# Optimization experiments

Measured on AMD Instinct MI355X. Metric: run time of the kernel, lower is better.

The kernel has to match this reference:

```python
import jax, jax.numpy as jnp
import numpy as np

HIDDEN = 2048
NUM_HEADS = 16
Q_LORA = 1536
KV_LORA = 512
QK_NOPE = 128
QK_ROPE = 64
V_HEAD = 128
EPS = 1e-6
QK_HEAD = QK_NOPE + QK_ROPE  # 192


def rmsnorm(x, w, eps=EPS):
    xf = x.astype(jnp.float32)
    var = jnp.mean(xf * xf, axis=-1, keepdims=True)
    return (w * (xf * jax.lax.rsqrt(var + eps)).astype(x.dtype))


def setup_inputs() -> dict:
    key = jax.random.key(0)
    ks = jax.random.split(key, 8)
    B, S = 1, 2048
    hidden_states = jax.random.normal(ks[0], (B, S, HIDDEN), dtype=jnp.float32)
    # causal additive mask [B,1,S,S]
    causal = jnp.tril(jnp.ones((S, S), dtype=bool))
    attention_mask = jnp.where(causal, 0.0, -1e9).astype(jnp.float32)[None, None]
    s = lambda fan_in: 1.0 / np.sqrt(fan_in)
    Wqa = jax.random.normal(ks[1], (HIDDEN, Q_LORA), dtype=jnp.float32) * s(HIDDEN)
    gqa = jnp.ones((Q_LORA,), dtype=jnp.float32)
    Wqb = jax.random.normal(ks[2], (Q_LORA, NUM_HEADS * QK_HEAD), dtype=jnp.float32) * s(Q_LORA)
    Wkva = jax.random.normal(ks[3], (HIDDEN, KV_LORA + QK_ROPE), dtype=jnp.float32) * s(HIDDEN)
    gkva = jnp.ones((KV_LORA,), dtype=jnp.float32)
    Wkvb = jax.random.normal(ks[4], (KV_LORA, NUM_HEADS * (QK_NOPE + V_HEAD)), dtype=jnp.float32) * s(KV_LORA)
    Wo = jax.random.normal(ks[5], (NUM_HEADS * V_HEAD, HIDDEN), dtype=jnp.float32) * s(NUM_HEADS * V_HEAD)
    return {"hidden_states": hidden_states, "attention_mask": attention_mask,
            "Wqa": Wqa, "gqa": gqa, "Wqb": Wqb, "Wkva": Wkva, "gkva": gkva,
            "Wkvb": Wkvb, "Wo": Wo}


def reference(hidden_states, attention_mask, Wqa, gqa, Wqb, Wkva, gkva, Wkvb, Wo):
    B, S, _ = hidden_states.shape
    # Q path: low-rank down-proj + RMSNorm + up-proj
    q_c = rmsnorm(hidden_states @ Wqa, gqa)
    q = (q_c @ Wqb).reshape(B, S, NUM_HEADS, QK_HEAD).transpose(0, 2, 1, 3)  # [B,H,S,192]
    # KV path: joint down-proj, split latent and shared rope part
    kv_c = hidden_states @ Wkva  # [B,S,KV_LORA+ROPE]
    kv_a, k_rope = kv_c[..., :KV_LORA], kv_c[..., KV_LORA:]
    kv = (rmsnorm(kv_a, gkva) @ Wkvb).reshape(B, S, NUM_HEADS, QK_NOPE + V_HEAD)
    k_nope, v = kv[..., :QK_NOPE], kv[..., QK_NOPE:]
    # shared rope part broadcast across heads (no rotary actually applied in source)
    k_rope_b = jnp.broadcast_to(k_rope[:, :, None, :], (B, S, NUM_HEADS, QK_ROPE))
    k = jnp.concatenate([k_nope, k_rope_b], axis=-1).transpose(0, 2, 1, 3)  # [B,H,S,192]
    v = v.transpose(0, 2, 1, 3)  # [B,H,S,128]
    scale = 1.0 / np.sqrt(QK_HEAD)
    attn = jnp.einsum("bhqd,bhkd->bhqk", q, k) * scale
    attn = attn + attention_mask
    attn = jax.nn.softmax(attn.astype(jnp.float32), axis=-1).astype(v.dtype)
    out = jnp.einsum("bhqk,bhkd->bhqd", attn, v)  # [B,H,S,128]
    out = out.transpose(0, 2, 1, 3).reshape(B, S, NUM_HEADS * V_HEAD)
    return out @ Wo
```

## Files before the change

kernel.cpp:

```cpp
#include <hip/hip_runtime.h>
#include <hip/hip_bf16.h>

typedef __bf16 bf16;
typedef __bf16 bf16x8 __attribute__((ext_vector_type(8)));
typedef __bf16 bf16x4 __attribute__((ext_vector_type(4)));
typedef float f32x4 __attribute__((ext_vector_type(4)));

#define HIDDEN 2048
#define SEQ 2048
#define NH 16
#define QL 1536
#define KVL 512
#define SCALE_LOG2E 0.10411754631f

__device__ __forceinline__ void gload_lds16(const void* g, void* l) {
  typedef const __attribute__((address_space(1))) void* gp_t;
  typedef __attribute__((address_space(3))) void* lp_t;
  __builtin_amdgcn_global_load_lds((gp_t)(unsigned long long)g,
                                   (lp_t)(unsigned int)(unsigned long long)l, 16, 0, 0);
}

__device__ __forceinline__ float fexp2(float x) {
  float r; asm("v_exp_f32 %0, %1" : "=v"(r) : "v"(x)); return r;
}
__device__ __forceinline__ unsigned cvt_pk_bf16(float lo, float hi) {
  unsigned r; asm("v_cvt_pk_bf16_f32 %0, %1, %2" : "=v"(r) : "v"(lo), "v"(hi)); return r;
}

__global__ void k_prep(const float* __restrict__ hidden, bf16* __restrict__ Xb,
                       const float* __restrict__ Wqa, bf16* __restrict__ WqaT,
                       const float* __restrict__ Wqb, bf16* __restrict__ WqbT,
                       const float* __restrict__ Wkva, bf16* __restrict__ WkvaT,
                       const float* __restrict__ Wkvb, bf16* __restrict__ WkvbT,
                       const float* __restrict__ Wo, bf16* __restrict__ WoT) {
  __shared__ float tile[32][33];
  int b = blockIdx.x, tid = threadIdx.x;
  const float* W; bf16* Wt; int K, N, bx, by;
  if (b < 3072)       { W = Wqa;  Wt = WqaT;  K = 2048; N = 1536; int r = b;         bx = r % 48;  by = r / 48; }
  else if (b < 7680)  { W = Wqb;  Wt = WqbT;  K = 1536; N = 3072; int r = b - 3072;  bx = r % 96;  by = r / 96; }
  else if (b < 8832)  { W = Wkva; Wt = WkvaT; K = 2048; N = 576;  int r = b - 7680;  bx = r % 18;  by = r / 18; }
  else if (b < 10880) { W = Wkvb; Wt = WkvbT; K = 512;  N = 4096; int r = b - 8832;  bx = r % 128; by = r / 128; }
  else if (b < 14976) { W = Wo;   Wt = WoT;   K = 2048; N = 2048; int r = b - 10880; bx = r % 64;  by = r / 64; }
  else {
    int r = b - 14976;
    int base = (r * 256 + tid) * 4;
    float4 v = *(const float4*)(hidden + base);
    bf16x4 o = { (bf16)v.x, (bf16)v.y, (bf16)v.z, (bf16)v.w };
    *(bf16x4*)(Xb + base) = o;
    return;
  }
  int n0 = bx * 32, k0 = by * 32, cc = tid & 31, rr = tid >> 5;
#pragma unroll
  for (int it = 0; it < 4; ++it) {
    int r = it * 8 + rr;
    tile[r][cc] = W[(size_t)(k0 + r) * N + n0 + cc];
  }
  __syncthreads();
#pragma unroll
  for (int it = 0; it < 4; ++it) {
    int r = it * 8 + rr;
    Wt[(size_t)(n0 + r) * K + k0 + cc] = (bf16)tile[cc][r];
  }
}

__device__ __forceinline__ void gemm_body(const bf16* __restrict__ A, const bf16* __restrict__ Bt,
                                          bf16* __restrict__ Cb, float* __restrict__ Cf,
                                          int N, int K, int m0, int n0, bf16* As, bf16* Bs) {
  int tid = threadIdx.x, lane = tid & 63, w = tid >> 6;
  int wr = w >> 1, wc = w & 1;
  int l15 = lane & 15, l4 = lane >> 4;
  f32x4 acc[4][4] = {};
  for (int k0 = 0; k0 < K; k0 += 64) {
#pragma unroll
    for (int i = 0; i < 4; ++i) {
      int c = w * 4 + i;
      int row = c * 8 + (lane >> 3);
      int col = (lane & 7) * 8;
      gload_lds16(&A[(size_t)(m0 + row) * K + k0 + col], &As[c * 512]);
      gload_lds16(&Bt[(size_t)(n0 + row) * K + k0 + col], &Bs[c * 512]);
    }
    __syncthreads();
#pragma unroll
    for (int kk = 0; kk < 2; ++kk) {
      bf16x8 af[4], bfr[4];
#pragma unroll
      for (int m = 0; m < 4; ++m)
        af[m] = *(const bf16x8*)&As[(wr * 64 + m * 16 + l15) * 64 + kk * 32 + l4 * 8];
#pragma unroll
      for (int n = 0; n < 4; ++n)
        bfr[n] = *(const bf16x8*)&Bs[(wc * 64 + n * 16 + l15) * 64 + kk * 32 + l4 * 8];
      __builtin_amdgcn_s_setprio(1);
#pragma unroll
      for (int m = 0; m < 4; ++m)
#pragma unroll
        for (int n = 0; n < 4; ++n)
          acc[m][n] = __builtin_amdgcn_mfma_f32_16x16x32_bf16(af[m], bfr[n], acc[m][n], 0, 0, 0);
      __builtin_amdgcn_s_setprio(0);
    }
    __syncthreads();
  }
#pragma unroll
  for (int m = 0; m < 4; ++m)
#pragma unroll
    for (int n = 0; n < 4; ++n)
#pragma unroll
      for (int r = 0; r < 4; ++r) {
        int grow = m0 + wr * 64 + m * 16 + l4 * 4 + r;
        int gcol = n0 + wc * 64 + n * 16 + l15;
        if (gcol < N) {
          float v = acc[m][n][r];
          if (Cf) Cf[(size_t)grow * N + gcol] = v;
          else Cb[(size_t)grow * N + gcol] = (bf16)v;
        }
      }
}

__global__ __launch_bounds__(256) void k_gemm(const bf16* __restrict__ A, const bf16* __restrict__ Bt,
                                              bf16* __restrict__ Cb, float* __restrict__ Cf,
                                              int N, int K) {
  __shared__ __align__(16) bf16 As[128 * 64];
  __shared__ __align__(16) bf16 Bs[128 * 64];
  gemm_body(A, Bt, Cb, Cf, N, K, blockIdx.x * 128, blockIdx.y * 128, As, Bs);
}

__global__ __launch_bounds__(256) void k_gemm_a(const bf16* __restrict__ Xb,
                                                const bf16* __restrict__ B1, const bf16* __restrict__ B2,
                                                float* __restrict__ C1, float* __restrict__ C2) {
  __shared__ __align__(16) bf16 As[128 * 64];
  __shared__ __align__(16) bf16 Bs[128 * 64];
  int by = blockIdx.y;
  if (by < 12) gemm_body(Xb, B1, nullptr, C1, 1536, 2048, blockIdx.x * 128, by * 128, As, Bs);
  else         gemm_body(Xb, B2, nullptr, C2, 576, 2048, blockIdx.x * 128, (by - 12) * 128, As, Bs);
}

__global__ __launch_bounds__(256) void k_gemm_b(const bf16* __restrict__ A1, const bf16* __restrict__ A2,
                                                const bf16* __restrict__ B1, const bf16* __restrict__ B2,
                                                bf16* __restrict__ C1, bf16* __restrict__ C2) {
  __shared__ __align__(16) bf16 As[128 * 64];
  __shared__ __align__(16) bf16 Bs[128 * 64];
  int by = blockIdx.y;
  if (by < 24) gemm_body(A1, B1, C1, nullptr, 3072, 1536, blockIdx.x * 128, by * 128, As, Bs);
  else         gemm_body(A2, B2, C2, nullptr, 4096, 512, blockIdx.x * 128, (by - 24) * 128, As, Bs);
}

__device__ inline float block_reduce_sum(float v, float* red) {
#pragma unroll
  for (int off = 1; off < 64; off <<= 1) v += __shfl_xor(v, off);
  int w = threadIdx.x >> 6;
  if ((threadIdx.x & 63) == 0) red[w] = v;
  __syncthreads();
  return red[0] + red[1] + red[2] + red[3];
}

__global__ void k_rms_all(const float* __restrict__ qa, const float* __restrict__ gq, bf16* __restrict__ qc,
                          const float* __restrict__ kvc, const float* __restrict__ gkv,
                          bf16* __restrict__ kvn, bf16* __restrict__ kr) {
  __shared__ float red[4];
  int b = blockIdx.x, tid = threadIdx.x;
  if (b < 2048) {
    int row = b;
    float v[6];
    float ss = 0.f;
#pragma unroll
    for (int j = 0; j < 6; ++j) {
      v[j] = qa[(size_t)row * QL + tid + j * 256];
      ss += v[j] * v[j];
    }
    float tot = block_reduce_sum(ss, red);
    float rs = rsqrtf(tot / (float)QL + 1e-6f);
#pragma unroll
    for (int j = 0; j < 6; ++j) {
      int c = tid + j * 256;
      qc[(size_t)row * QL + c] = (bf16)(v[j] * rs * gq[c]);
    }
  } else {
    int row = b - 2048;
    float v0 = kvc[(size_t)row * 576 + tid];
    float v1 = kvc[(size_t)row * 576 + tid + 256];
    float tot = block_reduce_sum(v0 * v0 + v1 * v1, red);
    float rs = rsqrtf(tot / (float)KVL + 1e-6f);
    kvn[(size_t)row * KVL + tid] = (bf16)(v0 * rs * gkv[tid]);
    kvn[(size_t)row * KVL + tid + 256] = (bf16)(v1 * rs * gkv[tid + 256]);
    if (tid < 64) kr[row * 64 + tid] = (bf16)kvc[(size_t)row * 576 + 512 + tid];
  }
}

__global__ void k_vt(const bf16* __restrict__ KVm, bf16* __restrict__ VT) {
  __shared__ bf16 tile[32][34];
  int b = blockIdx.x, tid = threadIdx.x;
  int h = b >> 8, rem = b & 255;
  int d0 = (rem >> 6) * 32, s0 = (rem & 63) * 32;
  int cc = tid & 31, rr = tid >> 5;
#pragma unroll
  for (int it = 0; it < 4; ++it) {
    int r = it * 8 + rr;
    tile[r][cc] = KVm[(size_t)(s0 + r) * 4096 + h * 256 + 128 + d0 + cc];
  }
  __syncthreads();
#pragma unroll
  for (int it = 0; it < 4; ++it) {
    int r = it * 8 + rr;
    VT[((size_t)(h * 128 + d0 + r)) * 2048 + s0 + cc] = tile[cc][r];
  }
}

__global__ __launch_bounds__(256) void k_attn(const bf16* __restrict__ Q, const bf16* __restrict__ KV,
                                              const bf16* __restrict__ KR, const bf16* __restrict__ VT,
                                              bf16* __restrict__ O) {
  __shared__ __align__(16) bf16 Ks[64 * 192];
  __shared__ __align__(16) bf16 Vt[128 * 64];
  __shared__ __align__(16) bf16 Ps[4 * 16 * 64];
  int bid = blockIdx.x;
  int h = bid & 15, i = bid >> 4;
  int qb = (i < 16) ? i : 47 - i;
  int q0 = qb * 64;
  int tid = threadIdx.x, lane = tid & 63, w = tid >> 6;
  int l15 = lane & 15, l4 = lane >> 4;
  int sw = (l15 & 7) << 4;
  char* PTw = (char*)Ps + w * 2048;
  const bf16* VTh = VT + (size_t)h * 128 * 2048;

  bf16x8 aq[6];
  int qrow = q0 + w * 16 + l15;
#pragma unroll
  for (int ks = 0; ks < 6; ++ks)
    aq[ks] = *(const bf16x8*)&Q[(size_t)qrow * 3072 + h * 192 + ks * 32 + l4 * 8];

  f32x4 oacc[8] = {};
  float mrun = -1e30f, lrun = 0.f;
  int nt = qb + 1;
  for (int t = 0; t < nt; ++t) {
#pragma unroll
    for (int it = 0; it < 6; ++it) {
      int idx = it * 256 + tid;
      int r = idx / 24, gg = idx - r * 24;
      int c = gg ^ (r & 7);
      const bf16* src = (c < 16) ? &KV[(size_t)(t * 64 + r) * 4096 + h * 256 + c * 8]
                                 : &KR[(size_t)(t * 64 + r) * 64 + (c - 16) * 8];
      gload_lds16(src, (char*)Ks + (it * 256 + w * 64) * 16);
    }
#pragma unroll
    for (int it = 0; it < 4; ++it) {
      int idx = it * 256 + tid;
      int d = idx >> 3, cc = idx & 7, c = cc ^ (d & 7);
      gload_lds16(&VTh[(size_t)d * 2048 + t * 64 + c * 8], (char*)Vt + (it * 256 + w * 64) * 16);
    }
    __syncthreads();

    f32x4 sacc[4] = {};
    __builtin_amdgcn_s_setprio(1);
#pragma unroll
    for (int ks = 0; ks < 6; ++ks) {
      int co = (((ks << 2) + l4) << 4) ^ sw;
#pragma unroll
      for (int n = 0; n < 4; ++n) {
        bf16x8 ak = *(const bf16x8*)((char*)Ks + (n * 16 + l15) * 384 + co);
        sacc[n] = __builtin_amdgcn_mfma_f32_16x16x32_bf16(ak, aq[ks], sacc[n], 0, 0, 0);
      }
    }
    __builtin_amdgcn_s_setprio(0);

    bool maskt = (t == qb);
#pragma unroll
    for (int n = 0; n < 4; ++n)
#pragma unroll
      for (int r = 0; r < 4; ++r) {
        float v = sacc[n][r] * SCALE_LOG2E;
        if (maskt) {
          int kvp = t * 64 + n * 16 + l4 * 4 + r;
          if (kvp > qrow) v = -1e30f;
        }
        sacc[n][r] = v;
      }

    float mx = sacc[0][0];
#pragma unroll
    for (int n = 0; n < 4; ++n)
#pragma unroll
      for (int r = 0; r < 4; ++r) mx = fmaxf(mx, sacc[n][r]);
    mx = fmaxf(mx, __shfl_xor(mx, 16));
    mx = fmaxf(mx, __shfl_xor(mx, 32));
    if (__any(mx - mrun > 8.0f)) {
      float mn = fmaxf(mrun, mx);
      float al = fexp2(mrun - mn);
      mrun = mn;
      lrun *= al;
#pragma unroll
      for (int vf = 0; vf < 8; ++vf) oacc[vf] *= al;
    }
    float rsum = 0.f;
#pragma unroll
    for (int n = 0; n < 4; ++n) {
      float e0 = fexp2(sacc[n][0] - mrun);
      float e1 = fexp2(sacc[n][1] - mrun);
      float e2 = fexp2(sacc[n][2] - mrun);
      float e3 = fexp2(sacc[n][3] - mrun);
      rsum += (e0 + e1) + (e2 + e3);
      uint2 u;
      u.x = cvt_pk_bf16(e0, e1);
      u.y = cvt_pk_bf16(e2, e3);
      *(uint2*)(PTw + l15 * 128 + ((n * 32 + l4 * 8) ^ sw)) = u;
    }
    rsum += __shfl_xor(rsum, 16);
    rsum += __shfl_xor(rsum, 32);
    lrun += rsum;

    __builtin_amdgcn_s_setprio(1);
#pragma unroll
    for (int ks = 0; ks < 2; ++ks) {
      int co = (((ks << 2) + l4) << 4) ^ sw;
      bf16x8 ap = *(const bf16x8*)(PTw + l15 * 128 + co);
#pragma unroll
      for (int vf = 0; vf < 8; ++vf) {
        bf16x8 av = *(const bf16x8*)((char*)Vt + (vf * 16 + l15) * 128 + co);
        oacc[vf] = __builtin_amdgcn_mfma_f32_16x16x32_bf16(av, ap, oacc[vf], 0, 0, 0);
      }
    }
    __builtin_amdgcn_s_setprio(0);
    __syncthreads();
  }

  char* OTw = (char*)Ks + w * 4096;
  float inv = 1.0f / lrun;
#pragma unroll
  for (int vf = 0; vf < 8; ++vf) {
    unsigned ua = cvt_pk_bf16(oacc[vf][0] * inv, oacc[vf][1] * inv);
    unsigned ub = cvt_pk_bf16(oacc[vf][2] * inv, oacc[vf][3] * inv);
    int base = vf * 32 + l4 * 8;
    *(unsigned*)(OTw + l15 * 256 + ((base + 0) ^ sw)) = ua;
    *(unsigned*)(OTw + l15 * 256 + ((base + 4) ^ sw)) = ub;
  }
  int qq = lane >> 2, c0 = lane & 3;
  size_t obase = (size_t)(q0 + w * 16 + qq) * 2048 + h * 128;
#pragma unroll
  for (int ii = 0; ii < 4; ++ii) {
    int ck = ii * 4 + c0;
    bf16x8 v = *(const bf16x8*)(OTw + qq * 256 + ((ck * 16) ^ ((qq & 7) << 4)));
    *(bf16x8*)&O[obase + ck * 8] = v;
  }
}

extern "C" void kernel_launch(void* const* d_in, const int* in_sizes, int n_in,
                              void* d_out, int out_size, void* d_ws, size_t ws_size,
                              hipStream_t stream) {
  (void)in_sizes; (void)n_in; (void)out_size; (void)ws_size;
  const float* hidden = (const float*)d_in[0];
  const float* Wqa  = (const float*)d_in[2];
  const float* gqa  = (const float*)d_in[3];
  const float* Wqb  = (const float*)d_in[4];
  const float* Wkva = (const float*)d_in[5];
  const float* gkva = (const float*)d_in[6];
  const float* Wkvb = (const float*)d_in[7];
  const float* Wo   = (const float*)d_in[8];
  float* out = (float*)d_out;

  char* ws = (char*)d_ws;
  size_t off = 0;
  auto alloc = [&](size_t bytes) {
    char* p = ws + off;
    off += (bytes + 255) & ~(size_t)255;
    return p;
  };
  bf16* Xb     = (bf16*)alloc((size_t)SEQ * HIDDEN * 2);
  bf16* WqaT   = (bf16*)alloc((size_t)QL * HIDDEN * 2);
  bf16* WqbT   = (bf16*)alloc((size_t)3072 * QL * 2);
  bf16* WkvaT  = (bf16*)alloc((size_t)576 * HIDDEN * 2);
  bf16* WkvbT  = (bf16*)alloc((size_t)4096 * KVL * 2);
  bf16* WoT    = (bf16*)alloc((size_t)2048 * 2048 * 2);
  float* qa    = (float*)alloc((size_t)SEQ * QL * 4);
  float* kvc   = (float*)alloc((size_t)SEQ * 576 * 4);
  bf16* qc     = (bf16*)alloc((size_t)SEQ * QL * 2);
  bf16* kvn    = (bf16*)alloc((size_t)SEQ * KVL * 2);
  bf16* krope  = (bf16*)alloc((size_t)SEQ * 64 * 2);
  bf16* Qm     = (bf16*)alloc((size_t)SEQ * 3072 * 2);
  bf16* KVm    = (bf16*)alloc((size_t)SEQ * 4096 * 2);
  bf16* VTg    = (bf16*)alloc((size_t)NH * 128 * SEQ * 2);
  bf16* Om     = (bf16*)alloc((size_t)SEQ * 2048 * 2);

  k_prep<<<19072, 256, 0, stream>>>(hidden, Xb, Wqa, WqaT, Wqb, WqbT,
                                    Wkva, WkvaT, Wkvb, WkvbT, Wo, WoT);
  k_gemm_a<<<dim3(16, 17), 256, 0, stream>>>(Xb, WqaT, WkvaT, qa, kvc);
  k_rms_all<<<4096, 256, 0, stream>>>(qa, gqa, qc, kvc, gkva, kvn, krope);
  k_gemm_b<<<dim3(16, 56), 256, 0, stream>>>(qc, kvn, WqbT, WkvbT, Qm, KVm);
  k_vt<<<4096, 256, 0, stream>>>(KVm, VTg);
  k_attn<<<512, 256, 0, stream>>>(Qm, KVm, krope, VTg, Om);
  k_gemm<<<dim3(16, 16), 256, 0, stream>>>(Om, WoT, nullptr, out, 2048, 2048);
}
```

Measured before the change: 236.5 us.

## Split attention KV range across blocks with 128-row query tiles and combine kernel

The attention kernel now processes 128 query rows per block, two 16-row groups per wave, so each K tile loaded into shared memory is reused twice as much. Longer causal query blocks are split along the KV dimension into 2-4 chunks (split-KV). Each chunk writes its unnormalized partial output and per-row max/sum, and a new combine kernel merges them with log-sum-exp weights. This is meant to cut K/V load traffic and balance work across the 640 blocks. The cost is an extra kernel launch, partial outputs rounded to bf16, and more register pressure from the doubled accumulators.

```diff
diff --git a/kernel.cpp b/kernel.cpp
--- a/kernel.cpp
+++ b/kernel.cpp
@@ -206,30 +206,38 @@
 
 __global__ __launch_bounds__(256) void k_attn(const bf16* __restrict__ Q, const bf16* __restrict__ KV,
                                               const bf16* __restrict__ KR, const bf16* __restrict__ VT,
-                                              bf16* __restrict__ O) {
+                                              bf16* __restrict__ O,
+                                              bf16* __restrict__ Opart, float2* __restrict__ Ml) {
   __shared__ __align__(16) bf16 Ks[64 * 192];
   __shared__ __align__(16) bf16 Vt[128 * 64];
-  __shared__ __align__(16) bf16 Ps[4 * 16 * 64];
+  __shared__ __align__(16) bf16 Ps[4 * 2 * 16 * 64];
   int bid = blockIdx.x;
-  int h = bid & 15, i = bid >> 4;
-  int qb = (i < 16) ? i : 47 - i;
-  int q0 = qb * 64;
+  int h = bid & 15, cid = bid >> 4;
+  int qbp, ch, nc;
+  if (cid < 4)       { qbp = cid; ch = 0; nc = 1; }
+  else if (cid < 12) { int r = cid - 4;  qbp = 4 + (r >> 1);  ch = r & 1; nc = 2; }
+  else if (cid < 24) { int r = cid - 12; qbp = 8 + r / 3;     ch = r % 3; nc = 3; }
+  else               { int r = cid - 24; qbp = 12 + (r >> 2); ch = r & 3; nc = 4; }
+  int T = 2 * qbp + 2;
+  int t0 = ch * T / nc, t1 = (ch + 1) * T / nc;
+  int q0 = qbp * 128;
   int tid = threadIdx.x, lane = tid & 63, w = tid >> 6;
   int l15 = lane & 15, l4 = lane >> 4;
   int sw = (l15 & 7) << 4;
-  char* PTw = (char*)Ps + w * 2048;
+  char* PTw = (char*)Ps + w * 4096;
   const bf16* VTh = VT + (size_t)h * 128 * 2048;
 
-  bf16x8 aq[6];
-  int qrow = q0 + w * 16 + l15;
-#pragma unroll
-  for (int ks = 0; ks < 6; ++ks)
-    aq[ks] = *(const bf16x8*)&Q[(size_t)qrow * 3072 + h * 192 + ks * 32 + l4 * 8];
-
-  f32x4 oacc[8] = {};
-  float mrun = -1e30f, lrun = 0.f;
-  int nt = qb + 1;
-  for (int t = 0; t < nt; ++t) {
+  bf16x8 aq[2][6];
+  int qrow0 = q0 + w * 32 + l15;
+#pragma unroll
+  for (int g = 0; g < 2; ++g)
+#pragma unroll
+    for (int ks = 0; ks < 6; ++ks)
+      aq[g][ks] = *(const bf16x8*)&Q[(size_t)(qrow0 + g * 16) * 3072 + h * 192 + ks * 32 + l4 * 8];
+
+  f32x4 oacc[2][8] = {};
+  float mrun[2] = {-1e30f, -1e30f}, lrun[2] = {0.f, 0.f};
+  for (int t = t0; t < t1; ++t) {
 #pragma unroll
     for (int it = 0; it < 6; ++it) {
       int idx = it * 256 + tid;
@@ -247,7 +255,7 @@
     }
     __syncthreads();
 
-    f32x4 sacc[4] = {};
+    f32x4 s0[4] = {}, s1[4] = {};
     __builtin_amdgcn_s_setprio(1);
 #pragma unroll
     for (int ks = 0; ks < 6; ++ks) {
@@ -255,65 +263,72 @@
 #pragma unroll
       for (int n = 0; n < 4; ++n) {
         bf16x8 ak = *(const bf16x8*)((char*)Ks + (n * 16 + l15) * 384 + co);
-        sacc[n] = __builtin_amdgcn_mfma_f32_16x16x32_bf16(ak, aq[ks], sacc[n], 0, 0, 0);
+        s0[n] = __builtin_amdgcn_mfma_f32_16x16x32_bf16(ak, aq[0][ks], s0[n], 0, 0, 0);
+        s1[n] = __builtin_amdgcn_mfma_f32_16x16x32_bf16(ak, aq[1][ks], s1[n], 0, 0, 0);
       }
     }
     __builtin_amdgcn_s_setprio(0);
 
-    bool maskt = (t == qb);
-#pragma unroll
-    for (int n = 0; n < 4; ++n)
-#pragma unroll
-      for (int r = 0; r < 4; ++r) {
-        float v = sacc[n][r] * SCALE_LOG2E;
-        if (maskt) {
-          int kvp = t * 64 + n * 16 + l4 * 4 + r;
-          if (kvp > qrow) v = -1e30f;
+    bool maskt = (t >= 2 * qbp);
+#pragma unroll
+    for (int g = 0; g < 2; ++g) {
+      f32x4* sacc = g ? s1 : s0;
+      int qrow = qrow0 + g * 16;
+#pragma unroll
+      for (int n = 0; n < 4; ++n)
+#pragma unroll
+        for (int r = 0; r < 4; ++r) {
+          float v = sacc[n][r] * SCALE_LOG2E;
+          if (maskt) {
+            int kvp = t * 64 + n * 16 + l4 * 4 + r;
+            if (kvp > qrow) v = -1e30f;
+          }
+          sacc[n][r] = v;
         }
-        sacc[n][r] = v;
+      float mx = sacc[0][0];
+#pragma unroll
+      for (int n = 0; n < 4; ++n)
+#pragma unroll
+        for (int r = 0; r < 4; ++r) mx = fmaxf(mx, sacc[n][r]);
+      mx = fmaxf(mx, __shfl_xor(mx, 16));
+      mx = fmaxf(mx, __shfl_xor(mx, 32));
+      if (__any(mx - mrun[g] > 8.0f)) {
+        float mn = fmaxf(mrun[g], mx);
+        float al = fexp2(mrun[g] - mn);
+        mrun[g] = mn;
+        lrun[g] *= al;
+#pragma unroll
+        for (int vf = 0; vf < 8; ++vf) oacc[g][vf] *= al;
       }
-
-    float mx = sacc[0][0];
-#pragma unroll
-    for (int n = 0; n < 4; ++n)
-#pragma unroll
-      for (int r = 0; r < 4; ++r) mx = fmaxf(mx, sacc[n][r]);
-    mx = fmaxf(mx, __shfl_xor(mx, 16));
-    mx = fmaxf(mx, __shfl_xor(mx, 32));
-    if (__any(mx - mrun > 8.0f)) {
-      float mn = fmaxf(mrun, mx);
-      float al = fexp2(mrun - mn);
-      mrun = mn;
-      lrun *= al;
-#pragma unroll
-      for (int vf = 0; vf < 8; ++vf) oacc[vf] *= al;
-    }
-    float rsum = 0.f;
-#pragma unroll
-    for (int n = 0; n < 4; ++n) {
-      float e0 = fexp2(sacc[n][0] - mrun);
-      float e1 = fexp2(sacc[n][1] - mrun);
-      float e2 = fexp2(sacc[n][2] - mrun);
-      float e3 = fexp2(sacc[n][3] - mrun);
-      rsum += (e0 + e1) + (e2 + e3);
-      uint2 u;
-      u.x = cvt_pk_bf16(e0, e1);
-      u.y = cvt_pk_bf16(e2, e3);
-      *(uint2*)(PTw + l15 * 128 + ((n * 32 + l4 * 8) ^ sw)) = u;
-    }
-    rsum += __shfl_xor(rsum, 16);
-    rsum += __shfl_xor(rsum, 32);
-    lrun += rsum;
+      float rsum = 0.f;
+#pragma unroll
+      for (int n = 0; n < 4; ++n) {
+        float e0 = fexp2(sacc[n][0] - mrun[g]);
+        float e1 = fexp2(sacc[n][1] - mrun[g]);
+        float e2 = fexp2(sacc[n][2] - mrun[g]);
+        float e3 = fexp2(sacc[n][3] - mrun[g]);
+        rsum += (e0 + e1) + (e2 + e3);
+        uint2 u;
+        u.x = cvt_pk_bf16(e0, e1);
+        u.y = cvt_pk_bf16(e2, e3);
+        *(uint2*)(PTw + g * 2048 + l15 * 128 + ((n * 32 + l4 * 8) ^ sw)) = u;
+      }
+      rsum += __shfl_xor(rsum, 16);
+      rsum += __shfl_xor(rsum, 32);
+      lrun[g] += rsum;
+    }
 
     __builtin_amdgcn_s_setprio(1);
 #pragma unroll
     for (int ks = 0; ks < 2; ++ks) {
       int co = (((ks << 2) + l4) << 4) ^ sw;
-      bf16x8 ap = *(const bf16x8*)(PTw + l15 * 128 + co);
+      bf16x8 ap0 = *(const bf16x8*)(PTw + l15 * 128 + co);
+      bf16x8 ap1 = *(const bf16x8*)(PTw + 2048 + l15 * 128 + co);
 #pragma unroll
       for (int vf = 0; vf < 8; ++vf) {
         bf16x8 av = *(const bf16x8*)((char*)Vt + (vf * 16 + l15) * 128 + co);
-        oacc[vf] = __builtin_amdgcn_mfma_f32_16x16x32_bf16(av, ap, oacc[vf], 0, 0, 0);
+        oacc[0][vf] = __builtin_amdgcn_mfma_f32_16x16x32_bf16(av, ap0, oacc[0][vf], 0, 0, 0);
+        oacc[1][vf] = __builtin_amdgcn_mfma_f32_16x16x32_bf16(av, ap1, oacc[1][vf], 0, 0, 0);
       }
     }
     __builtin_amdgcn_s_setprio(0);
@@ -321,22 +336,62 @@
   }
 
   char* OTw = (char*)Ks + w * 4096;
-  float inv = 1.0f / lrun;
-#pragma unroll
-  for (int vf = 0; vf < 8; ++vf) {
-    unsigned ua = cvt_pk_bf16(oacc[vf][0] * inv, oacc[vf][1] * inv);
-    unsigned ub = cvt_pk_bf16(oacc[vf][2] * inv, oacc[vf][3] * inv);
-    int base = vf * 32 + l4 * 8;
-    *(unsigned*)(OTw + l15 * 256 + ((base + 0) ^ sw)) = ua;
-    *(unsigned*)(OTw + l15 * 256 + ((base + 4) ^ sw)) = ub;
-  }
-  int qq = lane >> 2, c0 = lane & 3;
-  size_t obase = (size_t)(q0 + w * 16 + qq) * 2048 + h * 128;
-#pragma unroll
-  for (int ii = 0; ii < 4; ++ii) {
-    int ck = ii * 4 + c0;
-    bf16x8 v = *(const bf16x8*)(OTw + qq * 256 + ((ck * 16) ^ ((qq & 7) << 4)));
-    *(bf16x8*)&O[obase + ck * 8] = v;
+#pragma unroll
+  for (int g = 0; g < 2; ++g) {
+    float inv = (nc == 1) ? 1.0f / lrun[g] : 1.0f;
+#pragma unroll
+    for (int vf = 0; vf < 8; ++vf) {
+      unsigned ua = cvt_pk_bf16(oacc[g][vf][0] * inv, oacc[g][vf][1] * inv);
+      unsigned ub = cvt_pk_bf16(oacc[g][vf][2] * inv, oacc[g][vf][3] * inv);
+      int base = vf * 32 + l4 * 8;
+      *(unsigned*)(OTw + l15 * 256 + ((base + 0) ^ sw)) = ua;
+      *(unsigned*)(OTw + l15 * 256 + ((base + 4) ^ sw)) = ub;
+    }
+    int qq = lane >> 2, c0 = lane & 3;
+    int row = w * 32 + g * 16 + qq;
+    bf16* dst = (nc == 1) ? &O[(size_t)(q0 + row) * 2048 + h * 128]
+                          : &Opart[(size_t)bid * 128 * 128 + (size_t)row * 128];
+#pragma unroll
+    for (int ii = 0; ii < 4; ++ii) {
+      int ck = ii * 4 + c0;
+      bf16x8 v = *(const bf16x8*)(OTw + qq * 256 + ((ck * 16) ^ ((qq & 7) << 4)));
+      *(bf16x8*)&dst[ck * 8] = v;
+    }
+    if (nc > 1 && l4 == 0)
+      Ml[bid * 128 + w * 32 + g * 16 + l15] = make_float2(mrun[g], lrun[g]);
+  }
+}
+
+__global__ __launch_bounds__(256) void k_comb(const bf16* __restrict__ Opart,
+                                              const float2* __restrict__ Ml,
+                                              bf16* __restrict__ O) {
+  int b = blockIdx.x, h = b & 15, qbp = 4 + (b >> 4);
+  int cid0, nc;
+  if (qbp < 8)       { cid0 = 4 + 2 * (qbp - 4);   nc = 2; }
+  else if (qbp < 12) { cid0 = 12 + 3 * (qbp - 8);  nc = 3; }
+  else               { cid0 = 24 + 4 * (qbp - 12); nc = 4; }
+  int tid = threadIdx.x;
+  int rr = tid >> 5, col = (tid & 31) * 4;
+#pragma unroll
+  for (int rp = 0; rp < 16; ++rp) {
+    int row = rp * 8 + rr;
+    float M = -1e30f;
+    for (int c = 0; c < nc; ++c) M = fmaxf(M, Ml[((cid0 + c) * 16 + h) * 128 + row].x);
+    float acc0 = 0.f, acc1 = 0.f, acc2 = 0.f, acc3 = 0.f, L = 0.f;
+    for (int c = 0; c < nc; ++c) {
+      int slot = (cid0 + c) * 16 + h;
+      float2 ml = Ml[slot * 128 + row];
+      float wgt = fexp2(ml.x - M);
+      L += wgt * ml.y;
+      bf16x4 v = *(const bf16x4*)&Opart[(size_t)slot * 128 * 128 + row * 128 + col];
+      acc0 += wgt * (float)v[0];
+      acc1 += wgt * (float)v[1];
+      acc2 += wgt * (float)v[2];
+      acc3 += wgt * (float)v[3];
+    }
+    float inv = 1.0f / L;
+    bf16x4 o = { (bf16)(acc0 * inv), (bf16)(acc1 * inv), (bf16)(acc2 * inv), (bf16)(acc3 * inv) };
+    *(bf16x4*)&O[(size_t)(qbp * 128 + row) * 2048 + h * 128 + col] = o;
   }
 }
 
@@ -376,6 +431,8 @@
   bf16* KVm    = (bf16*)alloc((size_t)SEQ * 4096 * 2);
   bf16* VTg    = (bf16*)alloc((size_t)NH * 128 * SEQ * 2);
   bf16* Om     = (bf16*)alloc((size_t)SEQ * 2048 * 2);
+  float2* Ml   = (float2*)alloc((size_t)640 * 128 * 8);
+  bf16* Opart  = (bf16*)qa;
 
   k_prep<<<19072, 256, 0, stream>>>(hidden, Xb, Wqa, WqaT, Wqb, WqbT,
                                     Wkva, WkvaT, Wkvb, WkvbT, Wo, WoT);
@@ -383,6 +440,7 @@
   k_rms_all<<<4096, 256, 0, stream>>>(qa, gqa, qc, kvc, gkva, kvn, krope);
   k_gemm_b<<<dim3(16, 56), 256, 0, stream>>>(qc, kvn, WqbT, WkvbT, Qm, KVm);
   k_vt<<<4096, 256, 0, stream>>>(KVm, VTg);
-  k_attn<<<512, 256, 0, stream>>>(Qm, KVm, krope, VTg, Om);
+  k_attn<<<640, 256, 0, stream>>>(Qm, KVm, krope, VTg, Om, Opart, Ml);
+  k_comb<<<192, 256, 0, stream>>>(Opart, Ml, Om);
   k_gemm<<<dim3(16, 16), 256, 0, stream>>>(Om, WoT, nullptr, out, 2048, 2048);
 }
```

Result: slower. 273.2 us (+15.5%).

## Split-K by two for the down-projection and output GEMMs, summing partials afterwards

Applied to the files above, without the earlier changes.

The first down-projection GEMM and the final output projection now each split their K dimension into two halves. The halves run as separate blocks and write fp32 partial tiles to separate buffers. The RMSNorm kernel adds the two partials for the down-projection, and a new elementwise kernel adds them for the output. The aim is to double the block count, since those GEMMs only launched about one block per CU, to improve occupancy and latency hiding. The cost is extra fp32 write and read traffic, one more kernel launch, and workspace aliasing of qa0/qa1 and KVm as scratch for the output partials.

```diff
diff --git a/kernel.cpp b/kernel.cpp
--- a/kernel.cpp
+++ b/kernel.cpp
@@ -65,19 +65,20 @@
 
 __device__ __forceinline__ void gemm_body(const bf16* __restrict__ A, const bf16* __restrict__ Bt,
                                           bf16* __restrict__ Cb, float* __restrict__ Cf,
-                                          int N, int K, int m0, int n0, bf16* As, bf16* Bs) {
+                                          int N, int Kfull, int kbase, int Klen,
+                                          int m0, int n0, bf16* As, bf16* Bs) {
   int tid = threadIdx.x, lane = tid & 63, w = tid >> 6;
   int wr = w >> 1, wc = w & 1;
   int l15 = lane & 15, l4 = lane >> 4;
   f32x4 acc[4][4] = {};
-  for (int k0 = 0; k0 < K; k0 += 64) {
+  for (int k0 = kbase; k0 < kbase + Klen; k0 += 64) {
 #pragma unroll
     for (int i = 0; i < 4; ++i) {
       int c = w * 4 + i;
       int row = c * 8 + (lane >> 3);
       int col = (lane & 7) * 8;
-      gload_lds16(&A[(size_t)(m0 + row) * K + k0 + col], &As[c * 512]);
-      gload_lds16(&Bt[(size_t)(n0 + row) * K + k0 + col], &Bs[c * 512]);
+      gload_lds16(&A[(size_t)(m0 + row) * Kfull + k0 + col], &As[c * 512]);
+      gload_lds16(&Bt[(size_t)(n0 + row) * Kfull + k0 + col], &Bs[c * 512]);
     }
     __syncthreads();
 #pragma unroll
@@ -115,22 +116,22 @@
       }
 }
 
-__global__ __launch_bounds__(256) void k_gemm(const bf16* __restrict__ A, const bf16* __restrict__ Bt,
-                                              bf16* __restrict__ Cb, float* __restrict__ Cf,
-                                              int N, int K) {
-  __shared__ __align__(16) bf16 As[128 * 64];
-  __shared__ __align__(16) bf16 Bs[128 * 64];
-  gemm_body(A, Bt, Cb, Cf, N, K, blockIdx.x * 128, blockIdx.y * 128, As, Bs);
-}
-
 __global__ __launch_bounds__(256) void k_gemm_a(const bf16* __restrict__ Xb,
                                                 const bf16* __restrict__ B1, const bf16* __restrict__ B2,
-                                                float* __restrict__ C1, float* __restrict__ C2) {
+                                                float* __restrict__ qa0, float* __restrict__ qa1,
+                                                float* __restrict__ kvc0, float* __restrict__ kvc1) {
   __shared__ __align__(16) bf16 As[128 * 64];
   __shared__ __align__(16) bf16 Bs[128 * 64];
   int by = blockIdx.y;
-  if (by < 12) gemm_body(Xb, B1, nullptr, C1, 1536, 2048, blockIdx.x * 128, by * 128, As, Bs);
-  else         gemm_body(Xb, B2, nullptr, C2, 576, 2048, blockIdx.x * 128, (by - 12) * 128, As, Bs);
+  if (by < 24) {
+    int yy = by >> 1, kh = by & 1;
+    gemm_body(Xb, B1, nullptr, kh ? qa1 : qa0, 1536, 2048, kh * 1024, 1024,
+              blockIdx.x * 128, yy * 128, As, Bs);
+  } else {
+    int r = by - 24, yy = r >> 1, kh = r & 1;
+    gemm_body(Xb, B2, nullptr, kh ? kvc1 : kvc0, 576, 2048, kh * 1024, 1024,
+              blockIdx.x * 128, yy * 128, As, Bs);
+  }
 }
 
 __global__ __launch_bounds__(256) void k_gemm_b(const bf16* __restrict__ A1, const bf16* __restrict__ A2,
@@ -139,8 +140,26 @@
   __shared__ __align__(16) bf16 As[128 * 64];
   __shared__ __align__(16) bf16 Bs[128 * 64];
   int by = blockIdx.y;
-  if (by < 24) gemm_body(A1, B1, C1, nullptr, 3072, 1536, blockIdx.x * 128, by * 128, As, Bs);
-  else         gemm_body(A2, B2, C2, nullptr, 4096, 512, blockIdx.x * 128, (by - 24) * 128, As, Bs);
+  if (by < 24) gemm_body(A1, B1, C1, nullptr, 3072, 1536, 0, 1536, blockIdx.x * 128, by * 128, As, Bs);
+  else         gemm_body(A2, B2, C2, nullptr, 4096, 512, 0, 512, blockIdx.x * 128, (by - 24) * 128, As, Bs);
+}
+
+__global__ __launch_bounds__(256) void k_gemm_sk(const bf16* __restrict__ A, const bf16* __restrict__ Bt,
+                                                 float* __restrict__ O0, float* __restrict__ O1) {
+  __shared__ __align__(16) bf16 As[128 * 64];
+  __shared__ __align__(16) bf16 Bs[128 * 64];
+  int by = blockIdx.y, nt = by >> 1, kh = by & 1;
+  gemm_body(A, Bt, nullptr, kh ? O1 : O0, 2048, 2048, kh * 1024, 1024,
+            blockIdx.x * 128, nt * 128, As, Bs);
+}
+
+__global__ void k_add(const float* __restrict__ O0, const float* __restrict__ O1,
+                      float* __restrict__ out) {
+  int base = (blockIdx.x * 256 + threadIdx.x) * 4;
+  float4 a = *(const float4*)(O0 + base);
+  float4 b = *(const float4*)(O1 + base);
+  float4 o = { a.x + b.x, a.y + b.y, a.z + b.z, a.w + b.w };
+  *(float4*)(out + base) = o;
 }
 
 __device__ inline float block_reduce_sum(float v, float* red) {
@@ -152,8 +171,10 @@
   return red[0] + red[1] + red[2] + red[3];
 }
 
-__global__ void k_rms_all(const float* __restrict__ qa, const float* __restrict__ gq, bf16* __restrict__ qc,
-                          const float* __restrict__ kvc, const float* __restrict__ gkv,
+__global__ void k_rms_all(const float* __restrict__ qa0, const float* __restrict__ qa1,
+                          const float* __restrict__ gq, bf16* __restrict__ qc,
+                          const float* __restrict__ kvc0, const float* __restrict__ kvc1,
+                          const float* __restrict__ gkv,
                           bf16* __restrict__ kvn, bf16* __restrict__ kr) {
   __shared__ float red[4];
   int b = blockIdx.x, tid = threadIdx.x;
@@ -163,7 +184,8 @@
     float ss = 0.f;
 #pragma unroll
     for (int j = 0; j < 6; ++j) {
-      v[j] = qa[(size_t)row * QL + tid + j * 256];
+      size_t idx = (size_t)row * QL + tid + j * 256;
+      v[j] = qa0[idx] + qa1[idx];
       ss += v[j] * v[j];
     }
     float tot = block_reduce_sum(ss, red);
@@ -175,13 +197,14 @@
     }
   } else {
     int row = b - 2048;
-    float v0 = kvc[(size_t)row * 576 + tid];
-    float v1 = kvc[(size_t)row * 576 + tid + 256];
+    size_t base = (size_t)row * 576;
+    float v0 = kvc0[base + tid] + kvc1[base + tid];
+    float v1 = kvc0[base + tid + 256] + kvc1[base + tid + 256];
     float tot = block_reduce_sum(v0 * v0 + v1 * v1, red);
     float rs = rsqrtf(tot / (float)KVL + 1e-6f);
     kvn[(size_t)row * KVL + tid] = (bf16)(v0 * rs * gkv[tid]);
     kvn[(size_t)row * KVL + tid + 256] = (bf16)(v1 * rs * gkv[tid + 256]);
-    if (tid < 64) kr[row * 64 + tid] = (bf16)kvc[(size_t)row * 576 + 512 + tid];
+    if (tid < 64) kr[row * 64 + tid] = (bf16)(kvc0[base + 512 + tid] + kvc1[base + 512 + tid]);
   }
 }
 
@@ -367,8 +390,10 @@
   bf16* WkvaT  = (bf16*)alloc((size_t)576 * HIDDEN * 2);
   bf16* WkvbT  = (bf16*)alloc((size_t)4096 * KVL * 2);
   bf16* WoT    = (bf16*)alloc((size_t)2048 * 2048 * 2);
-  float* qa    = (float*)alloc((size_t)SEQ * QL * 4);
-  float* kvc   = (float*)alloc((size_t)SEQ * 576 * 4);
+  float* qa0   = (float*)alloc((size_t)SEQ * QL * 4);
+  float* qa1   = (float*)alloc((size_t)SEQ * QL * 4);
+  float* kvc0  = (float*)alloc((size_t)SEQ * 576 * 4);
+  float* kvc1  = (float*)alloc((size_t)SEQ * 576 * 4);
   bf16* qc     = (bf16*)alloc((size_t)SEQ * QL * 2);
   bf16* kvn    = (bf16*)alloc((size_t)SEQ * KVL * 2);
   bf16* krope  = (bf16*)alloc((size_t)SEQ * 64 * 2);
@@ -376,13 +401,16 @@
   bf16* KVm    = (bf16*)alloc((size_t)SEQ * 4096 * 2);
   bf16* VTg    = (bf16*)alloc((size_t)NH * 128 * SEQ * 2);
   bf16* Om     = (bf16*)alloc((size_t)SEQ * 2048 * 2);
+  float* O0 = qa0;
+  float* O1 = (float*)KVm;
 
   k_prep<<<19072, 256, 0, stream>>>(hidden, Xb, Wqa, WqaT, Wqb, WqbT,
                                     Wkva, WkvaT, Wkvb, WkvbT, Wo, WoT);
-  k_gemm_a<<<dim3(16, 17), 256, 0, stream>>>(Xb, WqaT, WkvaT, qa, kvc);
-  k_rms_all<<<4096, 256, 0, stream>>>(qa, gqa, qc, kvc, gkva, kvn, krope);
+  k_gemm_a<<<dim3(16, 34), 256, 0, stream>>>(Xb, WqaT, WkvaT, qa0, qa1, kvc0, kvc1);
+  k_rms_all<<<4096, 256, 0, stream>>>(qa0, qa1, gqa, qc, kvc0, kvc1, gkva, kvn, krope);
   k_gemm_b<<<dim3(16, 56), 256, 0, stream>>>(qc, kvn, WqbT, WkvbT, Qm, KVm);
   k_vt<<<4096, 256, 0, stream>>>(KVm, VTg);
   k_attn<<<512, 256, 0, stream>>>(Qm, KVm, krope, VTg, Om);
-  k_gemm<<<dim3(16, 16), 256, 0, stream>>>(Om, WoT, nullptr, out, 2048, 2048);
-}
+  k_gemm_sk<<<dim3(16, 32), 256, 0, stream>>>(Om, WoT, O0, O1);
+  k_add<<<4096, 256, 0, stream>>>(O0, O1, out);
+}
```

New measurement: 228.7 us. 3.3% less time.
